# Kernel optimization log

Measured on AMD Instinct MI355X. Metric: run time of the kernel, lower is better.

Reference implementation:

```python
import jax, jax.numpy as jnp
import numpy as np

B, K, D, H, NIRREPS = 1024, 16, 1024, 16, 16  # batch, seq_len(=group n), input_dim, heads, n_irreps
HD = D // H


def setup_inputs() -> dict:
    key = jax.random.key(0)
    ks = jax.random.split(key, 10)
    s = 1.0 / np.sqrt(D)
    return {
        "x": jax.random.normal(ks[0], (B, K, D), jnp.float32),
        "projectors": jax.random.normal(ks[1], (NIRREPS, K, K), jnp.float32) * 0.25,
        "Wq": jax.random.normal(ks[2], (D, D), jnp.float32) * s,
        "bq": jnp.zeros((D,), jnp.float32),
        "Wk": jax.random.normal(ks[3], (D, D), jnp.float32) * s,
        "bk": jnp.zeros((D,), jnp.float32),
        "Wv": jax.random.normal(ks[4], (D, D), jnp.float32) * s,
        "bv": jnp.zeros((D,), jnp.float32),
        "Wo": jax.random.normal(ks[5], (D, D), jnp.float32) * s,
        "bo": jnp.zeros((D,), jnp.float32),
    }


def reference(x, projectors, Wq, bq, Wk, bk, Wv, bv, Wo, bo):
    b, k, d = x.shape
    hd = d // H
    # QKV projections -> [b, H, k, hd]
    def heads(t):
        return t.reshape(b, k, H, hd).transpose(0, 2, 1, 3)
    Q = heads(x @ Wq + bq)
    Kt = heads(x @ Wk + bk)
    V = heads(x @ Wv + bv)
    scale = jnp.asarray(1.0 / np.sqrt(hd), x.dtype)

    # Per-irrep: project Q/K/V along the seq axis with P, run masked-free softmax
    # attention on tiny k x k scores, accumulate over irreps (eval mode, no dropout).
    def body(acc, P):
        Qp = jnp.einsum('ij,bhjd->bhid', P, Q)
        Kp = jnp.einsum('ij,bhjd->bhid', P, Kt)
        Vp = jnp.einsum('ij,bhjd->bhid', P, V)
        scores = jnp.einsum('bhid,bhjd->bhij', Qp, Kp) * scale
        w = jax.nn.softmax(scores, axis=-1)
        return acc + jnp.einsum('bhij,bhjd->bhid', w, Vp), None

    total, _ = jax.lax.scan(body, jnp.zeros_like(V), projectors)
    # merge heads -> [b, k, d], then output projection
    out = total.transpose(0, 2, 1, 3).reshape(b, k, d) @ Wo + bo
    return out
```

## Files before the change

kernel.cpp:

```cpp
#include <hip/hip_runtime.h>


typedef unsigned short u16;
typedef unsigned int u32;
typedef __attribute__((ext_vector_type(8))) __bf16 bf16x8;
typedef __attribute__((ext_vector_type(4))) float f32x4;
typedef __attribute__((ext_vector_type(4))) u32 u32x4;
typedef __attribute__((ext_vector_type(4))) u16 u16x4;
typedef __attribute__((ext_vector_type(4))) float float4v;
typedef __attribute__((address_space(1))) void gvoid;
typedef __attribute__((address_space(3))) void svoid;

#define MFMA16(a, b, c) __builtin_amdgcn_mfma_f32_16x16x32_bf16(a, b, c, 0, 0, 0)

__device__ __forceinline__ u16 f2bf(float f) {
  u32 u = __builtin_bit_cast(u32, f);
  return (u16)((u + 0x7fffu + ((u >> 16) & 1u)) >> 16);
}
__device__ __forceinline__ float bf2f(u16 h) {
  u32 u = ((u32)h) << 16;
  return __builtin_bit_cast(float, u);
}
__device__ __forceinline__ float ld_bias(const void* p, int i, int isf32) {
  return isf32 ? ((const float*)p)[i] : bf2f(((const u16*)p)[i]);
}
__device__ __forceinline__ bf16x8 ld_frag(const u16* p) {
  u32x4 v = *reinterpret_cast<const u32x4*>(p);
  return __builtin_bit_cast(bf16x8, v);
}
__device__ __forceinline__ bf16x8 ld_frag_lo(const u16* p, int lane) {
  u32x4 v = {0u, 0u, 0u, 0u};
  if (lane < 32) v = *reinterpret_cast<const u32x4*>(p);
  return __builtin_bit_cast(bf16x8, v);
}
__device__ __forceinline__ void async16(const u16* g, u16* l) {
  __builtin_amdgcn_global_load_lds((gvoid*)g, (svoid*)l, 16, 0, 0);
}

__device__ __forceinline__ bf16x8 c2frag(f32x4 v, int lane) {
  const u32 p01 = ((u32)f2bf(v[1]) << 16) | (u32)f2bf(v[0]);
  const u32 p23 = ((u32)f2bf(v[3]) << 16) | (u32)f2bf(v[2]);
  const int base = (lane & 15) + ((lane & 16) << 1);
  u32x4 o;
  o[0] = (u32)__shfl((int)p01, base);
  o[1] = (u32)__shfl((int)p23, base);
  o[2] = (u32)__shfl((int)p01, base + 16);
  o[3] = (u32)__shfl((int)p23, base + 16);
  if (lane >= 32) o = (u32x4){0u, 0u, 0u, 0u};
  return __builtin_bit_cast(bf16x8, o);
}

__global__ __launch_bounds__(1024) void detect_dtype(const u32* __restrict__ x,
                                                     int* __restrict__ flag) {
  const int tid = threadIdx.x;
  int cnt = 0;
#pragma unroll
  for (int q = 0; q < 4; ++q) {
    const u32x4 v = ((const u32x4*)x)[q * 1024 + tid];
#pragma unroll
    for (int j = 0; j < 4; ++j) {
      const u32 e = (v[j] >> 23) & 0xffu;
      cnt += (e >= 64u && e <= 191u) ? 1 : 0;
    }
  }
  __shared__ int sred[16];
  for (int o = 32; o; o >>= 1) cnt += __shfl_down(cnt, o);
  if ((tid & 63) == 0) sred[tid >> 6] = cnt;
  __syncthreads();
  if (tid == 0) {
    int t = 0;
#pragma unroll
    for (int i = 0; i < 16; ++i) t += sred[i];
    flag[0] = (t > 8192) ? 1 : 0;
  }
}

__global__ __launch_bounds__(256) void convert_x(const void* __restrict__ src,
                                                 u16* __restrict__ dst,
                                                 const int* __restrict__ flag) {
  const int i4 = blockIdx.x * 256 + threadIdx.x;
  if (*flag) {
    const float4v v = ((const float4v*)src)[i4];
    u16x4 o;
#pragma unroll
    for (int j = 0; j < 4; ++j) o[j] = f2bf(v[j]);
    ((u16x4*)dst)[i4] = o;
  } else {
    ((u16x4*)dst)[i4] = ((const u16x4*)src)[i4];
  }
}

__global__ __launch_bounds__(256) void transpose_conv(
    const void* __restrict__ w0, const void* __restrict__ w1,
    const void* __restrict__ w2, const void* __restrict__ w3,
    u16* __restrict__ d0, u16* __restrict__ d1, u16* __restrict__ d2,
    u16* __restrict__ d3, const int* __restrict__ flag) {
  __shared__ u16 tile[32][33];
  const int z = blockIdx.z;
  const void* src = (z == 0) ? w0 : (z == 1) ? w1 : (z == 2) ? w2 : w3;
  u16* dst = (z == 0) ? d0 : (z == 1) ? d1 : (z == 2) ? d2 : d3;
  const int isf32 = *flag;
  const int tx = threadIdx.x & 31;
  const int ty = (threadIdx.x >> 5) * 4;
  const int bx = blockIdx.x * 32;
  const int by = blockIdx.y * 32;
#pragma unroll
  for (int r = 0; r < 4; ++r) {
    const int idx = (by + ty + r) * 1024 + bx + tx;
    tile[ty + r][tx] = isf32 ? f2bf(((const float*)src)[idx]) : ((const u16*)src)[idx];
  }
  __syncthreads();
#pragma unroll
  for (int r = 0; r < 4; ++r)
    dst[(bx + ty + r) * 1024 + by + tx] = tile[tx][ty + r];
}

template <int MODE>
__global__ __launch_bounds__(512, 2) void gemm256(
    const u16* __restrict__ X, const u16* __restrict__ Wt,
    const void* __restrict__ b0, const void* __restrict__ b1,
    const void* __restrict__ b2, void* __restrict__ o0, u16* __restrict__ o1,
    u16* __restrict__ o2, const int* __restrict__ flag) {
  __shared__ alignas(16) u16 sm[65536];
  const int tid = threadIdx.x;
  const int wave = tid >> 6, lane = tid & 63;
  const int fr = lane & 15, fq = lane >> 4;
  const int wm = wave >> 2, wn = wave & 3;
  const int isf32 = *flag;

  const int nwg = gridDim.x;
  const int per = nwg >> 3;
  const int bid = blockIdx.x;
  const int wg = (bid & 7) * per + (bid >> 3);
  const int m0 = (wg & 63) << 8;
  const int n0 = (wg >> 6) << 8;

  const int gl = ((tid & 7) ^ ((tid >> 3) & 7)) * 8;
  const u16* aS = X + (size_t)(m0 + (tid >> 3)) * 1024 + gl;
  const u16* bS = Wt + (size_t)(n0 + (tid >> 3)) * 1024 + gl;
  u16* dA = sm + wave * 512;
  u16* dB = sm + 16384 + wave * 512;

  const u16* aR = sm + (wm * 128 + fr) * 64;
  const u16* bR = sm + 16384 + (wn * 64 + fr) * 64;
  const int g0 = (fq ^ (fr & 7)) * 8;
  const int g1 = ((fq ^ (fr & 7)) ^ 4) * 8;

  f32x4 acc[2][4][4] = {};
  bf16x8 af[2][4][2], bf[4][2];

#define STG_A(BUF, H, KT)                                                     \
  do {                                                                        \
    async16(aS + (H * 128) * 1024 + (KT), dA + (BUF)*32768 + (H)*8192);       \
    async16(aS + (H * 128 + 64) * 1024 + (KT),                                \
            dA + (BUF)*32768 + (H)*8192 + 4096);                              \
  } while (0)
#define STG_B(BUF, H, KT)                                                     \
  do {                                                                        \
    async16(bS + (H * 128) * 1024 + (KT), dB + (BUF)*32768 + (H)*8192);       \
    async16(bS + (H * 128 + 64) * 1024 + (KT),                                \
            dB + (BUF)*32768 + (H)*8192 + 4096);                              \
  } while (0)
#define LDA_ALL(CH, KH, BUF)                                                  \
  do {                                                                        \
    af[CH][0][KH] = ld_frag(aR + (BUF)*32768 + (CH)*4096 + ((KH) ? g1 : g0)); \
    af[CH][1][KH] =                                                           \
        ld_frag(aR + (BUF)*32768 + (CH)*4096 + 1024 + ((KH) ? g1 : g0));      \
    af[CH][2][KH] =                                                           \
        ld_frag(aR + (BUF)*32768 + (CH)*4096 + 2048 + ((KH) ? g1 : g0));      \
    af[CH][3][KH] =                                                           \
        ld_frag(aR + (BUF)*32768 + (CH)*4096 + 3072 + ((KH) ? g1 : g0));      \
  } while (0)
#define LDB_ALL(KH, BUF)                                                      \
  do {                                                                        \
    bf[0][KH] = ld_frag(bR + (BUF)*32768 + ((KH) ? g1 : g0));                 \
    bf[1][KH] = ld_frag(bR + (BUF)*32768 + 1024 + ((KH) ? g1 : g0));          \
    bf[2][KH] = ld_frag(bR + (BUF)*32768 + 2048 + ((KH) ? g1 : g0));          \
    bf[3][KH] = ld_frag(bR + (BUF)*32768 + 3072 + ((KH) ? g1 : g0));          \
  } while (0)
#define MM1(CH, FI, KH)                                                       \
  acc[CH][FI][0] = MFMA16(af[CH][FI][KH], bf[0][KH], acc[CH][FI][0]);         \
  acc[CH][FI][1] = MFMA16(af[CH][FI][KH], bf[1][KH], acc[CH][FI][1]);         \
  acc[CH][FI][2] = MFMA16(af[CH][FI][KH], bf[2][KH], acc[CH][FI][2]);         \
  acc[CH][FI][3] = MFMA16(af[CH][FI][KH], bf[3][KH], acc[CH][FI][3]);
#define MM(CH, KH)                                                            \
  do {                                                                        \
    __builtin_amdgcn_s_setprio(1);                                            \
    MM1(CH, 0, KH) MM1(CH, 1, KH) MM1(CH, 2, KH) MM1(CH, 3, KH)               \
    __builtin_amdgcn_s_setprio(0);                                            \
  } while (0)
#define BARR                                                                  \
  __builtin_amdgcn_s_barrier();                                               \
  __builtin_amdgcn_sched_barrier(0)
#define WAITV_IMM(N) asm volatile("s_waitcnt vmcnt(" #N ")" ::: "memory")
#define WAITV(N) WAITV_IMM(N)
#define WAITL asm volatile("s_waitcnt lgkmcnt(0)" ::: "memory")
#define SCHED __builtin_amdgcn_sched_barrier(0)

#define PHASES(DO_STG, KOF, W1V, DO_W4)                                       \
  do {                                                                        \
                                                                      \
    LDA_ALL(0, 0, 0);                                                         \
    LDB_ALL(0, 0);                                                            \
    LDA_ALL(1, 0, 0);                                                         \
    BARR;                                                                     \
    MM(0, 0);                                                                 \
    BARR;                                                                     \
                     \
    LDA_ALL(0, 1, 0);                                                         \
    LDA_ALL(1, 1, 0);                                                         \
    BARR;                                                                     \
    MM(1, 0);                                                                 \
    WAITL;                                                                    \
    SCHED;                                                                    \
    BARR;                                                                     \
                                      \
    LDB_ALL(1, 0);                                                            \
    if (DO_STG) STG_A(0, 0, (KOF) + 128);                                     \
    BARR;                                                                     \
    MM(0, 1);                                                                 \
    BARR;                                                                     \
           \
    if (DO_STG) {                                                             \
      STG_A(0, 1, (KOF) + 128);                                               \
      STG_B(0, 0, (KOF) + 128);                                               \
      STG_B(0, 1, (KOF) + 128);                                               \
    }                                                                         \
    BARR;                                                                     \
    MM(1, 1);                                                                 \
    WAITV(W1V);                                                               \
    SCHED;                                                                    \
    BARR;                                                                     \
                                                                      \
    LDA_ALL(0, 0, 1);                                                         \
    LDB_ALL(0, 1);                                                            \
    LDA_ALL(1, 0, 1);                                                         \
    BARR;                                                                     \
    MM(0, 0);                                                                 \
    BARR;                                                                     \
                                                  \
    LDA_ALL(0, 1, 1);                                                         \
    LDA_ALL(1, 1, 1);                                                         \
    BARR;                                                                     \
    MM(1, 0);                                                                 \
    WAITL;                                                                    \
    SCHED;                                                                    \
    BARR;                                                                     \
                                      \
    LDB_ALL(1, 1);                                                            \
    if (DO_STG) STG_A(1, 0, (KOF) + 192);                                     \
    BARR;                                                                     \
    MM(0, 1);                                                                 \
    BARR;                                                                     \
                                        \
    if (DO_STG) {                                                             \
      STG_A(1, 1, (KOF) + 192);                                               \
      STG_B(1, 0, (KOF) + 192);                                               \
      STG_B(1, 1, (KOF) + 192);                                               \
    }                                                                         \
    BARR;                                                                     \
    MM(1, 1);                                                                 \
    if (DO_W4) {                                                              \
      WAITV(8);                                                               \
      SCHED;                                                                  \
    }                                                                         \
    BARR;                                                                     \
  } while (0)

  STG_A(0, 0, 0);
  STG_A(0, 1, 0);
  STG_B(0, 0, 0);
  STG_B(0, 1, 0);
  STG_A(1, 0, 64);
  STG_A(1, 1, 64);
  STG_B(1, 0, 64);
  STG_B(1, 1, 64);
  WAITV(8);
  BARR;

  for (int it = 0; it < 7; ++it) {
    const int kof = it * 128;
    PHASES(1, kof, 8, 1);
  }
  PHASES(0, 0, 0, 0);

  if constexpr (MODE == 0) {
    const int q = n0 >> 10;
    const int nb = (n0 & 1023) + wn * 64;
    const void* bp = (q == 0) ? b0 : ((q == 1) ? b1 : b2);
    u16* q0 = (u16*)o0;
#pragma unroll
    for (int ch = 0; ch < 2; ++ch)
#pragma unroll
      for (int fi = 0; fi < 4; ++fi) {
        const int mbase = m0 + wm * 128 + ch * 64 + fi * 16;
        const int bidx = mbase >> 4;
#pragma unroll
        for (int bj = 0; bj < 4; ++bj) {
          const int nl = nb + bj * 16 + fr;
          const int h = nl >> 6, d = nl & 63;
          const float bias = ld_bias(bp, nl, isf32);
          const int bh = bidx * 16 + h;
          if (q == 2) {
            u16x4 pk;
#pragma unroll
            for (int r = 0; r < 4; ++r) pk[r] = f2bf(acc[ch][fi][bj][r] + bias);
            *reinterpret_cast<u16x4*>(&o2[(bh * 64 + d) * 16 + fq * 4]) = pk;
          } else {
            u16* dstq = (q == 0) ? q0 : o1;
#pragma unroll
            for (int r = 0; r < 4; ++r)
              dstq[(bh * 16 + fq * 4 + r) * 64 + d] =
                  f2bf(acc[ch][fi][bj][r] + bias);
          }
        }
      }
  } else {
#pragma unroll
    for (int ch = 0; ch < 2; ++ch)
#pragma unroll
      for (int fi = 0; fi < 4; ++fi) {
        const int m = m0 + wm * 128 + ch * 64 + fi * 16 + fq * 4;
#pragma unroll
        for (int bj = 0; bj < 4; ++bj) {
          const int n = n0 + wn * 64 + bj * 16 + fr;
          const float bias = ld_bias(b0, n, isf32);
          if (isf32) {
#pragma unroll
            for (int r = 0; r < 4; ++r)
              ((float*)o0)[(m + r) * 1024 + n] = acc[ch][fi][bj][r] + bias;
          } else {
#pragma unroll
            for (int r = 0; r < 4; ++r)
              ((u16*)o0)[(m + r) * 1024 + n] = f2bf(acc[ch][fi][bj][r] + bias);
          }
        }
      }
  }
#undef STG_A
#undef STG_B
#undef LDA_ALL
#undef LDB_ALL
#undef MM1
#undef MM
#undef BARR
#undef WAITV_IMM
#undef WAITV
#undef WAITL
#undef SCHED
#undef PHASES
}

__global__ __launch_bounds__(256) void attn_kernel(
    const u16* __restrict__ Qb, const u16* __restrict__ Kb, const u16* __restrict__ Vt,
    const void* __restrict__ P, u16* __restrict__ Tb,
    const int* __restrict__ flag) {
  __shared__ alignas(16) u16 Pl[4096];
  __shared__ alignas(16) u16 Ptl[4096];
  const int tid = threadIdx.x;
  const int isf32 = *flag;
#pragma unroll
  for (int i = 0; i < 16; ++i) {
    const int idx = i * 256 + tid;
    const u16 v = isf32 ? f2bf(((const float*)P)[idx]) : ((const u16*)P)[idx];
    Pl[idx] = v;
    const int p = idx >> 8, rc = idx & 255, rr = rc >> 4, cc = rc & 15;
    Ptl[(p << 8) + (cc << 4) + rr] = v;
  }
  __syncthreads();

  const int wave = tid >> 6, lane = tid & 63;
  const int bh = blockIdx.x * 4 + wave;
  const int fr = lane & 15, fq = lane >> 4;

  const u16* qb = Qb + bh * 1024;
  const u16* kb = Kb + bh * 1024;
  const u16* vb = Vt + bh * 1024;

  const bf16x8 qf0 = ld_frag(qb + fr * 64 + fq * 8);
  const bf16x8 qf1 = ld_frag(qb + fr * 64 + 32 + fq * 8);
  const bf16x8 kf0 = ld_frag(kb + fr * 64 + fq * 8);
  const bf16x8 kf1 = ld_frag(kb + fr * 64 + 32 + fq * 8);
  f32x4 S = {0.f, 0.f, 0.f, 0.f};
  S = MFMA16(qf0, kf0, S);
  S = MFMA16(qf1, kf1, S);
#pragma unroll
  for (int r = 0; r < 4; ++r) S[r] *= 0.125f;
  const bf16x8 St = c2frag(S, lane);

  f32x4 Mt = {0.f, 0.f, 0.f, 0.f};
#pragma unroll 4
  for (int p = 0; p < 16; ++p) {
    const bf16x8 pl = ld_frag_lo(Pl + (p << 8) + fr * 16 + fq * 8, lane);
    const bf16x8 pt = ld_frag_lo(Ptl + (p << 8) + fr * 16 + fq * 8, lane);
    f32x4 z = {0.f, 0.f, 0.f, 0.f};
    const f32x4 ApT = MFMA16(St, pl, z);
    const f32x4 BpT = MFMA16(pl, c2frag(ApT, lane), z);
    float e[4], s = 0.f;
#pragma unroll
    for (int r = 0; r < 4; ++r) {
      e[r] = __expf(BpT[r]);
      s += e[r];
    }
    s += __shfl_xor(s, 16);
    s += __shfl_xor(s, 32);
    const float rs = __frcp_rn(s);
    f32x4 w;
#pragma unroll
    for (int r = 0; r < 4; ++r) w[r] = e[r] * rs;
    Mt = MFMA16(pt, c2frag(w, lane), Mt);
  }

  const bf16x8 mb = c2frag(Mt, lane);

  const int b = bh >> 4, h = bh & 15;
  u16* outp = Tb + (b * 16 + fr) * 1024 + h * 64;
#pragma unroll
  for (int dt = 0; dt < 4; ++dt) {
    const bf16x8 vf = ld_frag_lo(vb + (dt * 16 + fr) * 16 + fq * 8, lane);
    f32x4 z = {0.f, 0.f, 0.f, 0.f};
    const f32x4 ot = MFMA16(vf, mb, z);
    u16x4 pk;
#pragma unroll
    for (int r = 0; r < 4; ++r) pk[r] = f2bf(ot[r]);
    *reinterpret_cast<u16x4*>(&outp[dt * 16 + fq * 4]) = pk;
  }
}

extern "C" void kernel_launch(void* const* d_in, const int* in_sizes, int n_in,
                              void* d_out, int out_size, void* d_ws, size_t ws_size,
                              hipStream_t stream) {
  const void* x = d_in[0];
  const void* proj = d_in[1];
  const void* Wq = d_in[2];
  const void* bq = d_in[3];
  const void* Wk = d_in[4];
  const void* bk = d_in[5];
  const void* Wv = d_in[6];
  const void* bv = d_in[7];
  const void* Wo = d_in[8];
  const void* bo = d_in[9];

  char* ws = (char*)d_ws;
  int* flag = (int*)ws;          ws += 256;
  u16* WtQKV = (u16*)ws;         ws += (size_t)3072 * 1024 * 2;
  u16* WtO   = (u16*)ws;         ws += (size_t)1024 * 1024 * 2;
  u16* Xb    = (u16*)ws;         ws += (size_t)16384 * 1024 * 2;
  u16* Qbuf  = (u16*)ws;         ws += (size_t)16384 * 1024 * 2;
  u16* Kbuf  = (u16*)ws;         ws += (size_t)16384 * 1024 * 2;
  u16* Vtb   = (u16*)ws;         ws += (size_t)16384 * 1024 * 2;
  u16* Tbuf  = (u16*)ws;         ws += (size_t)16384 * 1024 * 2;

  detect_dtype<<<1, 1024, 0, stream>>>((const u32*)x, flag);
  convert_x<<<16384, 256, 0, stream>>>(x, Xb, flag);
  transpose_conv<<<dim3(32, 32, 4), 256, 0, stream>>>(
      Wq, Wk, Wv, Wo, WtQKV, WtQKV + 1024 * 1024, WtQKV + 2 * 1024 * 1024, WtO, flag);

  gemm256<0><<<dim3(768), 512, 0, stream>>>(
      Xb, WtQKV, bq, bk, bv, Qbuf, Kbuf, Vtb, flag);
  attn_kernel<<<4096, 256, 0, stream>>>(Qbuf, Kbuf, Vtb, proj, Tbuf, flag);
  gemm256<1><<<dim3(256), 512, 0, stream>>>(
      Tbuf, WtO, bo, nullptr, nullptr, d_out, nullptr, nullptr, flag);
}
```

Before: 358.9 us.

## Make QKV GEMM persistent over three N tiles and merge preprocessing kernels

Folds the x conversion and the weight transpose/convert into one preprocess launch. The QKV GEMM now runs 256 workgroups, each looping over three 256-wide N tiles. While the current tile finishes its epilogue, the next tile's first K slabs are prefetched into the pipeline. This removes a kernel launch and the per-tile pipeline fill. In exchange, each workgroup holds its A rows across N tiles and there are fewer waves (one per CU) to hide the epilogue stores.

```diff
diff --git a/kernel.cpp b/kernel.cpp
--- a/kernel.cpp
+++ b/kernel.cpp
@@ -75,47 +75,49 @@
   }
 }
 
-__global__ __launch_bounds__(256) void convert_x(const void* __restrict__ src,
-                                                 u16* __restrict__ dst,
-                                                 const int* __restrict__ flag) {
-  const int i4 = blockIdx.x * 256 + threadIdx.x;
-  if (*flag) {
-    const float4v v = ((const float4v*)src)[i4];
-    u16x4 o;
-#pragma unroll
-    for (int j = 0; j < 4; ++j) o[j] = f2bf(v[j]);
-    ((u16x4*)dst)[i4] = o;
-  } else {
-    ((u16x4*)dst)[i4] = ((const u16x4*)src)[i4];
-  }
-}
-
-__global__ __launch_bounds__(256) void transpose_conv(
+__global__ __launch_bounds__(256) void preprocess(
+    const void* __restrict__ src_x, u16* __restrict__ dst_x,
     const void* __restrict__ w0, const void* __restrict__ w1,
     const void* __restrict__ w2, const void* __restrict__ w3,
     u16* __restrict__ d0, u16* __restrict__ d1, u16* __restrict__ d2,
     u16* __restrict__ d3, const int* __restrict__ flag) {
   __shared__ u16 tile[32][33];
-  const int z = blockIdx.z;
-  const void* src = (z == 0) ? w0 : (z == 1) ? w1 : (z == 2) ? w2 : w3;
-  u16* dst = (z == 0) ? d0 : (z == 1) ? d1 : (z == 2) ? d2 : d3;
+  const int bid = blockIdx.x;
+  const int tid = threadIdx.x;
   const int isf32 = *flag;
-  const int tx = threadIdx.x & 31;
-  const int ty = (threadIdx.x >> 5) * 4;
-  const int bx = blockIdx.x * 32;
-  const int by = blockIdx.y * 32;
-#pragma unroll
-  for (int r = 0; r < 4; ++r) {
-    const int idx = (by + ty + r) * 1024 + bx + tx;
-    tile[ty + r][tx] = isf32 ? f2bf(((const float*)src)[idx]) : ((const u16*)src)[idx];
-  }
-  __syncthreads();
-#pragma unroll
-  for (int r = 0; r < 4; ++r)
-    dst[(bx + ty + r) * 1024 + by + tx] = tile[tx][ty + r];
-}
-
-template <int MODE>
+  if (bid < 16384) {
+    const int i4 = bid * 256 + tid;
+    if (isf32) {
+      const float4v v = ((const float4v*)src_x)[i4];
+      u16x4 o;
+#pragma unroll
+      for (int j = 0; j < 4; ++j) o[j] = f2bf(v[j]);
+      ((u16x4*)dst_x)[i4] = o;
+    } else {
+      ((u16x4*)dst_x)[i4] = ((const u16x4*)src_x)[i4];
+    }
+  } else {
+    const int r = bid - 16384;
+    const int z = r >> 10;
+    const void* src = (z == 0) ? w0 : (z == 1) ? w1 : (z == 2) ? w2 : w3;
+    u16* dst = (z == 0) ? d0 : (z == 1) ? d1 : (z == 2) ? d2 : d3;
+    const int tx = tid & 31;
+    const int ty = (tid >> 5) * 4;
+    const int bx = (r & 31) * 32;
+    const int by = ((r >> 5) & 31) * 32;
+#pragma unroll
+    for (int q = 0; q < 4; ++q) {
+      const int idx = (by + ty + q) * 1024 + bx + tx;
+      tile[ty + q][tx] = isf32 ? f2bf(((const float*)src)[idx]) : ((const u16*)src)[idx];
+    }
+    __syncthreads();
+#pragma unroll
+    for (int q = 0; q < 4; ++q)
+      dst[(bx + ty + q) * 1024 + by + tx] = tile[tx][ty + q];
+  }
+}
+
+template <int MODE, int TILES>
 __global__ __launch_bounds__(512, 2) void gemm256(
     const u16* __restrict__ X, const u16* __restrict__ Wt,
     const void* __restrict__ b0, const void* __restrict__ b1,
@@ -133,11 +135,11 @@
   const int bid = blockIdx.x;
   const int wg = (bid & 7) * per + (bid >> 3);
   const int m0 = (wg & 63) << 8;
-  const int n0 = (wg >> 6) << 8;
+  const int ng0 = (wg >> 6) * TILES;
 
   const int gl = ((tid & 7) ^ ((tid >> 3) & 7)) * 8;
   const u16* aS = X + (size_t)(m0 + (tid >> 3)) * 1024 + gl;
-  const u16* bS = Wt + (size_t)(n0 + (tid >> 3)) * 1024 + gl;
+  const u16* bS0 = Wt + (size_t)(ng0 * 256 + (tid >> 3)) * 1024 + gl;
   u16* dA = sm + wave * 512;
   u16* dB = sm + 16384 + wave * 512;
 
@@ -155,10 +157,10 @@
     async16(aS + (H * 128 + 64) * 1024 + (KT),                                \
             dA + (BUF)*32768 + (H)*8192 + 4096);                              \
   } while (0)
-#define STG_B(BUF, H, KT)                                                     \
-  do {                                                                        \
-    async16(bS + (H * 128) * 1024 + (KT), dB + (BUF)*32768 + (H)*8192);       \
-    async16(bS + (H * 128 + 64) * 1024 + (KT),                                \
+#define STG_B(SRC, BUF, H, KT)                                                \
+  do {                                                                        \
+    async16((SRC) + (H * 128) * 1024 + (KT), dB + (BUF)*32768 + (H)*8192);    \
+    async16((SRC) + (H * 128 + 64) * 1024 + (KT),                             \
             dB + (BUF)*32768 + (H)*8192 + 4096);                              \
   } while (0)
 #define LDA_ALL(CH, KH, BUF)                                                  \
@@ -197,7 +199,7 @@
 #define WAITL asm volatile("s_waitcnt lgkmcnt(0)" ::: "memory")
 #define SCHED __builtin_amdgcn_sched_barrier(0)
 
-#define PHASES(DO_STG, KOF, W1V, DO_W4)                                       \
+#define PHASES(STG, BSRC, AKA, AKB, BKA, BKB)                                 \
   do {                                                                        \
                                                                       \
     LDA_ALL(0, 0, 0);                                                         \
@@ -206,7 +208,7 @@
     BARR;                                                                     \
     MM(0, 0);                                                                 \
     BARR;                                                                     \
-                     \
+                                                  \
     LDA_ALL(0, 1, 0);                                                         \
     LDA_ALL(1, 1, 0);                                                         \
     BARR;                                                                     \
@@ -214,21 +216,25 @@
     WAITL;                                                                    \
     SCHED;                                                                    \
     BARR;                                                                     \
-                                      \
+                                           \
     LDB_ALL(1, 0);                                                            \
-    if (DO_STG) STG_A(0, 0, (KOF) + 128);                                     \
+    if (STG) STG_A(0, 0, AKA);                                                \
     BARR;                                                                     \
     MM(0, 1);                                                                 \
     BARR;                                                                     \
            \
-    if (DO_STG) {                                                             \
-      STG_A(0, 1, (KOF) + 128);                                               \
-      STG_B(0, 0, (KOF) + 128);                                               \
-      STG_B(0, 1, (KOF) + 128);                                               \
+    if (STG) {                                                                \
+      STG_A(0, 1, AKA);                                                       \
+      STG_B(BSRC, 0, 0, BKA);                                                 \
+      STG_B(BSRC, 0, 1, BKA);                                                 \
     }                                                                         \
     BARR;                                                                     \
     MM(1, 1);                                                                 \
-    WAITV(W1V);                                                               \
+    if (STG) {                                                                \
+      WAITV(8);                                                               \
+    } else {                                                                  \
+      WAITV(0);                                                               \
+    }                                                                         \
     SCHED;                                                                    \
     BARR;                                                                     \
                                                                       \
@@ -246,21 +252,21 @@
     WAITL;                                                                    \
     SCHED;                                                                    \
     BARR;                                                                     \
-                                      \
+                                           \
     LDB_ALL(1, 1);                                                            \
-    if (DO_STG) STG_A(1, 0, (KOF) + 192);                                     \
+    if (STG) STG_A(1, 0, AKB);                                                \
     BARR;                                                                     \
     MM(0, 1);                                                                 \
     BARR;                                                                     \
-                                        \
-    if (DO_STG) {                                                             \
-      STG_A(1, 1, (KOF) + 192);                                               \
-      STG_B(1, 0, (KOF) + 192);                                               \
-      STG_B(1, 1, (KOF) + 192);                                               \
+      \
+    if (STG) {                                                                \
+      STG_A(1, 1, AKB);                                                       \
+      STG_B(BSRC, 1, 0, BKB);                                                 \
+      STG_B(BSRC, 1, 1, BKB);                                                 \
     }                                                                         \
     BARR;                                                                     \
     MM(1, 1);                                                                 \
-    if (DO_W4) {                                                              \
+    if (STG) {                                                                \
       WAITV(8);                                                               \
       SCHED;                                                                  \
     }                                                                         \
@@ -269,73 +275,92 @@
 
   STG_A(0, 0, 0);
   STG_A(0, 1, 0);
-  STG_B(0, 0, 0);
-  STG_B(0, 1, 0);
+  STG_B(bS0, 0, 0, 0);
+  STG_B(bS0, 0, 1, 0);
   STG_A(1, 0, 64);
   STG_A(1, 1, 64);
-  STG_B(1, 0, 64);
-  STG_B(1, 1, 64);
+  STG_B(bS0, 1, 0, 64);
+  STG_B(bS0, 1, 1, 64);
   WAITV(8);
   BARR;
 
-  for (int it = 0; it < 7; ++it) {
-    const int kof = it * 128;
-    PHASES(1, kof, 8, 1);
-  }
-  PHASES(0, 0, 0, 0);
-
-  if constexpr (MODE == 0) {
-    const int q = n0 >> 10;
-    const int nb = (n0 & 1023) + wn * 64;
-    const void* bp = (q == 0) ? b0 : ((q == 1) ? b1 : b2);
-    u16* q0 = (u16*)o0;
-#pragma unroll
-    for (int ch = 0; ch < 2; ++ch)
-#pragma unroll
-      for (int fi = 0; fi < 4; ++fi) {
-        const int mbase = m0 + wm * 128 + ch * 64 + fi * 16;
-        const int bidx = mbase >> 4;
-#pragma unroll
-        for (int bj = 0; bj < 4; ++bj) {
-          const int nl = nb + bj * 16 + fr;
-          const int h = nl >> 6, d = nl & 63;
-          const float bias = ld_bias(bp, nl, isf32);
-          const int bh = bidx * 16 + h;
-          if (q == 2) {
-            u16x4 pk;
-#pragma unroll
-            for (int r = 0; r < 4; ++r) pk[r] = f2bf(acc[ch][fi][bj][r] + bias);
-            *reinterpret_cast<u16x4*>(&o2[(bh * 64 + d) * 16 + fq * 4]) = pk;
-          } else {
-            u16* dstq = (q == 0) ? q0 : o1;
-#pragma unroll
-            for (int r = 0; r < 4; ++r)
-              dstq[(bh * 16 + fq * 4 + r) * 64 + d] =
-                  f2bf(acc[ch][fi][bj][r] + bias);
+#pragma unroll 1
+  for (int t = 0; t < TILES; ++t) {
+    const u16* bSt = bS0 + (size_t)t * 256 * 1024;
+    const u16* bSn = bSt + 256 * 1024;
+    for (int it = 0; it < 7; ++it) {
+      const int kof = it * 128;
+      PHASES(1, bSt, kof + 128, kof + 192, kof + 128, kof + 192);
+    }
+    if (t + 1 < TILES) {
+      PHASES(1, bSn, 0, 64, 0, 64);
+    } else {
+      PHASES(0, bSt, 0, 64, 0, 64);
+    }
+
+    const int n0 = (ng0 + t) << 8;
+    if constexpr (MODE == 0) {
+      const int q = n0 >> 10;
+      const int nb = (n0 & 1023) + wn * 64;
+      const void* bp = (q == 0) ? b0 : ((q == 1) ? b1 : b2);
+      u16* q0 = (u16*)o0;
+#pragma unroll
+      for (int ch = 0; ch < 2; ++ch)
+#pragma unroll
+        for (int fi = 0; fi < 4; ++fi) {
+          const int mbase = m0 + wm * 128 + ch * 64 + fi * 16;
+          const int bidx = mbase >> 4;
+#pragma unroll
+          for (int bj = 0; bj < 4; ++bj) {
+            const int nl = nb + bj * 16 + fr;
+            const int h = nl >> 6, d = nl & 63;
+            const float bias = ld_bias(bp, nl, isf32);
+            const int bh = bidx * 16 + h;
+            if (q == 2) {
+              u16x4 pk;
+#pragma unroll
+              for (int r = 0; r < 4; ++r) pk[r] = f2bf(acc[ch][fi][bj][r] + bias);
+              *reinterpret_cast<u16x4*>(&o2[(bh * 64 + d) * 16 + fq * 4]) = pk;
+            } else {
+              u16* dstq = (q == 0) ? q0 : o1;
+#pragma unroll
+              for (int r = 0; r < 4; ++r)
+                dstq[(bh * 16 + fq * 4 + r) * 64 + d] =
+                    f2bf(acc[ch][fi][bj][r] + bias);
+            }
           }
         }
-      }
-  } else {
-#pragma unroll
-    for (int ch = 0; ch < 2; ++ch)
-#pragma unroll
-      for (int fi = 0; fi < 4; ++fi) {
-        const int m = m0 + wm * 128 + ch * 64 + fi * 16 + fq * 4;
-#pragma unroll
-        for (int bj = 0; bj < 4; ++bj) {
-          const int n = n0 + wn * 64 + bj * 16 + fr;
-          const float bias = ld_bias(b0, n, isf32);
-          if (isf32) {
-#pragma unroll
-            for (int r = 0; r < 4; ++r)
-              ((float*)o0)[(m + r) * 1024 + n] = acc[ch][fi][bj][r] + bias;
-          } else {
-#pragma unroll
-            for (int r = 0; r < 4; ++r)
-              ((u16*)o0)[(m + r) * 1024 + n] = f2bf(acc[ch][fi][bj][r] + bias);
+    } else {
+#pragma unroll
+      for (int ch = 0; ch < 2; ++ch)
+#pragma unroll
+        for (int fi = 0; fi < 4; ++fi) {
+          const int m = m0 + wm * 128 + ch * 64 + fi * 16 + fq * 4;
+#pragma unroll
+          for (int bj = 0; bj < 4; ++bj) {
+            const int n = n0 + wn * 64 + bj * 16 + fr;
+            const float bias = ld_bias(b0, n, isf32);
+            if (isf32) {
+#pragma unroll
+              for (int r = 0; r < 4; ++r)
+                ((float*)o0)[(m + r) * 1024 + n] = acc[ch][fi][bj][r] + bias;
+            } else {
+#pragma unroll
+              for (int r = 0; r < 4; ++r)
+                ((u16*)o0)[(m + r) * 1024 + n] = f2bf(acc[ch][fi][bj][r] + bias);
+            }
           }
         }
-      }
+    }
+    if (t + 1 < TILES) {
+#pragma unroll
+      for (int a1 = 0; a1 < 2; ++a1)
+#pragma unroll
+        for (int a2 = 0; a2 < 4; ++a2)
+#pragma unroll
+          for (int a3 = 0; a3 < 4; ++a3)
+            acc[a1][a2][a3] = (f32x4){0.f, 0.f, 0.f, 0.f};
+    }
   }
 #undef STG_A
 #undef STG_B
@@ -452,13 +477,13 @@
   u16* Tbuf  = (u16*)ws;         ws += (size_t)16384 * 1024 * 2;
 
   detect_dtype<<<1, 1024, 0, stream>>>((const u32*)x, flag);
-  convert_x<<<16384, 256, 0, stream>>>(x, Xb, flag);
-  transpose_conv<<<dim3(32, 32, 4), 256, 0, stream>>>(
-      Wq, Wk, Wv, Wo, WtQKV, WtQKV + 1024 * 1024, WtQKV + 2 * 1024 * 1024, WtO, flag);
-
-  gemm256<0><<<dim3(768), 512, 0, stream>>>(
+  preprocess<<<20480, 256, 0, stream>>>(
+      x, Xb, Wq, Wk, Wv, Wo, WtQKV, WtQKV + 1024 * 1024,
+      WtQKV + 2 * 1024 * 1024, WtO, flag);
+
+  gemm256<0, 3><<<dim3(256), 512, 0, stream>>>(
       Xb, WtQKV, bq, bk, bv, Qbuf, Kbuf, Vtb, flag);
   attn_kernel<<<4096, 256, 0, stream>>>(Qbuf, Kbuf, Vtb, proj, Tbuf, flag);
-  gemm256<1><<<dim3(256), 512, 0, stream>>>(
+  gemm256<1, 1><<<dim3(256), 512, 0, stream>>>(
       Tbuf, WtO, bo, nullptr, nullptr, d_out, nullptr, nullptr, flag);
 }
```

New measurement: 633.1 us. 1.76x slower.
